# Kernel optimization log

Hardware: AMD Instinct MI355X
Metric: run time of the kernel (lower is better)

Reference implementation:

```python
import jax, jax.numpy as jnp
import numpy as np

B = 4096
D_IN = 1024
H1 = 2048
H2 = 1024
E = 7          # num_experts, forced by broadcasting in source
T = 2          # num_tasks
NS = 7         # scene dimension of S
EMB_ROWS = 10
EMB_DIM = 16


def setup_inputs() -> dict:
    key = jax.random.key(0)
    ks = jax.random.split(key, 8)
    x = jax.random.normal(ks[0], (B, D_IN), dtype=jnp.float32)
    scene = jax.random.randint(ks[1], (B,), 0, E)
    # Expert MLP params, stacked over experts: Linear(D_IN->H1)+ReLU, Linear(H1->H2)+ReLU
    W1 = jax.random.normal(ks[2], (E, D_IN, H1), dtype=jnp.float32) * (1.0 / np.sqrt(D_IN))
    b1 = jnp.zeros((E, H1), dtype=jnp.float32)
    W2 = jax.random.normal(ks[3], (E, H1, H2), dtype=jnp.float32) * (1.0 / np.sqrt(H1))
    b2 = jnp.zeros((E, H2), dtype=jnp.float32)
    # Routing tensor S: [7, input_dim+16, num_experts] (xavier-like init)
    S = jax.random.normal(ks[4], (NS, D_IN + EMB_DIM, E), dtype=jnp.float32) * 0.02
    scene_emb = jax.random.normal(ks[5], (EMB_ROWS, EMB_DIM), dtype=jnp.float32)
    return {"x": x, "scene": scene, "W1": W1, "b1": b1, "W2": W2, "b2": b2,
            "S": S, "scene_emb": scene_emb}


def _forward(x, scene, W1, b1, W2, b2, S, scene_emb):
    # Experts (vectorized over the E expert MLPs): [B,E,H2]
    h = jax.nn.relu(jnp.einsum('bd,edh->beh', x, W1) + b1)
    experts_out = jax.nn.relu(jnp.einsum('beh,eho->beo', h, W2) + b2)

    se = scene_emb[scene]                       # [B,16]
    xc = jnp.concatenate([x, se], axis=-1)      # [B, D_IN+16]
    G = jnp.einsum('bd,sde->bse', xc, S)        # [B, 7, E]
    G = jnp.transpose(G, (0, 2, 1))             # [B, E, 7]
    G = jax.nn.softmax(G, axis=-1)

    logG = jnp.log(G)                           # [B, E, 7]
    q = jnp.sum(jnp.log(G * 7.0) / 7.0, axis=-1)  # [B, E]

    KG = jnp.eye(E, dtype=x.dtype)
    ses = KG[scene][:, None, :]                 # [B, 1, E]

    _, pi = jax.lax.top_k(jnp.sum(ses * logG, axis=-1), 6)  # [B,6]
    _, qi = jax.lax.top_k(q, 6)                              # [B,6]
    select = ((KG[pi].sum(axis=1) + KG[qi].sum(axis=1)) > 0).astype(x.dtype)  # [B,E]

    gate = jax.nn.softmax(jnp.sum(G * ses, axis=-1), axis=-1) * select  # [B,E]
    out = jnp.einsum('be,bed->bd', gate, experts_out)                    # [B,H2]
    # self.gate ModuleList is unused in the source forward; each task output is identical
    return jnp.stack([out] * T, axis=0)         # [T, B, H2]


def reference(x, scene, W1, b1, W2, b2, S, scene_emb):
    return _forward(x, scene, W1, b1, W2, b2, S, scene_emb)
```

## Files before the change

### kernel.cpp

```cpp
#include <hip/hip_runtime.h>
#include <hip/hip_bf16.h>

typedef unsigned short u16;
typedef __bf16 bf8 __attribute__((ext_vector_type(8)));
typedef float f4 __attribute__((ext_vector_type(4)));

__device__ __forceinline__ u16 f2bf(float f) {
    unsigned int u = __float_as_uint(f);
    u = (u + 0x7fffu + ((u >> 16) & 1u)) >> 16;
    return (u16)u;
}

__device__ __forceinline__ void gload16(const u16* g, u16* l) {
    __builtin_amdgcn_global_load_lds((const __attribute__((address_space(1))) void*)g,
                                     (__attribute__((address_space(3))) void*)l, 16, 0, 0);
}

__global__ void transpose_cvt_kernel(const float* __restrict__ in, u16* __restrict__ out,
                                     int R, int C) {
    __shared__ u16 t[64][71];
    int e = blockIdx.z;
    int c0 = blockIdx.x * 64, r0 = blockIdx.y * 64;
    int tid = threadIdx.x;
    const float* ip = in + (size_t)e * R * C;
    u16* op = out + (size_t)e * R * C;
#pragma unroll
    for (int k = 0; k < 16; ++k) {
        int idx = k * 256 + tid;
        int r = idx >> 6, c = idx & 63;
        t[c][r] = f2bf(ip[(size_t)(r0 + r) * C + c0 + c]);
    }
    __syncthreads();
#pragma unroll
    for (int k = 0; k < 8; ++k) {
        int c = k * 8 + (tid >> 5);
        int rr = (tid & 31) * 2;
        ushort2 v = make_ushort2(t[c][rr], t[c][rr + 1]);
        *(ushort2*)(op + (size_t)(c0 + c) * R + r0 + rr) = v;
    }
}

__global__ void transpose_S_kernel(const float* __restrict__ S, float* __restrict__ ST) {
    int idx = blockIdx.x * 256 + threadIdx.x;
    if (idx >= 1040 * 52) return;
    int d = idx / 52, c = idx % 52;
    ST[idx] = (c < 49) ? S[(c / 7) * 7280 + d * 7 + (c % 7)] : 0.f;
}

__global__ void gating_kernel(const float* __restrict__ x, const int* __restrict__ scene,
                              const float* __restrict__ ST, const float* __restrict__ semb,
                              float* __restrict__ gate, u16* __restrict__ xb) {
    __shared__ float xc[4][1040];
    __shared__ float Lsh[4][49];
    int wv = threadIdx.x >> 6, lane = threadIdx.x & 63;
    int row = blockIdx.x * 4 + wv;
    float* xcw = xc[wv];
    const float* xr = x + (size_t)row * 1024;
    for (int d = lane; d < 1024; d += 64) xcw[d] = xr[d];
    int sc = scene[row];
    if (lane < 16) xcw[1024 + lane] = semb[sc * 16 + lane];
    __syncthreads();

    u16* xrow = xb + (size_t)row * 1024;
    for (int d = lane * 4; d < 1024; d += 256) {
        ushort4 o;
        o.x = f2bf(xcw[d]);     o.y = f2bf(xcw[d + 1]);
        o.z = f2bf(xcw[d + 2]); o.w = f2bf(xcw[d + 3]);
        *(ushort4*)(xrow + d) = o;
    }

    if (lane < 49) {
        const float* STp = ST + lane;
        float a0 = 0.f, a1 = 0.f, a2 = 0.f, a3 = 0.f;
        for (int d = 0; d < 1040; d += 4) {
            a0 += xcw[d]     * STp[d * 52];
            a1 += xcw[d + 1] * STp[d * 52 + 52];
            a2 += xcw[d + 2] * STp[d * 52 + 104];
            a3 += xcw[d + 3] * STp[d * 52 + 156];
        }
        Lsh[wv][lane] = (a0 + a1) + (a2 + a3);
    }
    __syncthreads();

    if (lane == 0) {
        float logG[7][7], Gsc[7], piS[7], qS[7];
        for (int e = 0; e < 7; e++) {
            float L[7];
            float m = -1e30f;
            for (int s = 0; s < 7; s++) { L[s] = Lsh[wv][s * 7 + e]; m = fmaxf(m, L[s]); }
            float sum = 0.f;
            for (int s = 0; s < 7; s++) sum += expf(L[s] - m);
            float lse = m + logf(sum);
            float qs = 0.f;
            for (int s = 0; s < 7; s++) { logG[e][s] = L[s] - lse; qs += logG[e][s]; }
            piS[e] = logG[e][sc];
            qS[e] = qs;
            Gsc[e] = expf(logG[e][sc]);
        }
        int epi = 0, eqi = 0; float bp = piS[0], bq = qS[0];
        for (int e = 1; e < 7; e++) {
            if (piS[e] <= bp) { bp = piS[e]; epi = e; }
            if (qS[e]  <= bq) { bq = qS[e];  eqi = e; }
        }
        float mg = -1e30f;
        for (int e = 0; e < 7; e++) mg = fmaxf(mg, Gsc[e]);
        float sum = 0.f;
        float ex[7];
        for (int e = 0; e < 7; e++) { ex[e] = expf(Gsc[e] - mg); sum += ex[e]; }
        float inv = 1.f / sum;
        for (int e = 0; e < 7; e++) {
            float g = ex[e] * inv;
            if (e == epi && e == eqi) g = 0.f;
            gate[row * 7 + e] = g;
        }
    }
}

template<bool G2>
__global__ __launch_bounds__(512, 2) void gemm8p_kernel(
    const u16* __restrict__ Abase, const u16* __restrict__ Bbase,
    const float* __restrict__ bias, const float* __restrict__ gate,
    void* __restrict__ outp)
{
    constexpr int M = 4096;
    constexpr int K = G2 ? 2048 : 1024;
    constexpr int N = G2 ? 1024 : 2048;
    constexpr int NT = K / 64;
    constexpr int LOG2NT = G2 ? 5 : 4;

    extern __shared__ u16 lds[];

    const int tid = threadIdx.x;
    const int lane = tid & 63;
    const int wid = tid >> 6;
    const int wr = wid >> 2, wc = wid & 3;
    const int ln15 = lane & 15, lnk = (lane >> 4) * 8;

    int bm, bn, e0, nE, grp;
    if constexpr (G2) {
        int id = blockIdx.x;
        int xcd = id & 7, slot = id >> 3;
        grp = xcd & 1;
        bn = slot & 3;
        bm = (slot >> 2) * 4 + (xcd >> 1);
        e0 = grp * 4; nE = grp ? 3 : 4;
    } else {
        int xcd = blockIdx.x & 7, slot = blockIdx.x >> 3;
        bn = slot >> 2;
        bm = (slot & 3) * 8 + xcd;
        e0 = 0; nE = 7; grp = 0;
    }
    const int NTtot = nE * NT;

    const int sr = tid >> 3;
    const int sc = (tid & 7) * 8;

    auto stageA = [&](int gt, int buf) {
#pragma unroll
        for (int l = 0; l < 2; ++l) {
            int r = l * 64 + sr;
            int cs = sc ^ ((r & 7) << 3);
            const u16* g = Abase + (G2 ? (size_t)(e0 + (gt >> LOG2NT)) * M * K : (size_t)0)
                         + (size_t)(bm * 128 + r) * K + (gt & (NT - 1)) * 64 + cs;
            gload16(g, lds + buf * 24576 + l * 4096 + tid * 8);
        }
    };
    auto stageB = [&](int gt, int buf, int h) {
#pragma unroll
        for (int l = 0; l < 2; ++l) {
            int rb = h * 128 + l * 64 + sr;
            int cs = sc ^ ((rb & 7) << 3);
            const u16* g = Bbase + (size_t)(e0 + (gt >> LOG2NT)) * N * K
                         + (size_t)(bn * 256 + rb) * K + (gt & (NT - 1)) * 64 + cs;
            gload16(g, lds + buf * 24576 + 8192 + h * 8192 + l * 4096 + tid * 8);
        }
    };
    auto aoff = [&](int mi, int ks) {
        int r = wr * 64 + mi * 16 + ln15;
        int c = ks * 32 + lnk;
        return r * 64 + (c ^ ((r & 7) << 3));
    };
    auto boff = [&](int ni, int ks) {
        int rb = wc * 64 + ni * 16 + ln15;
        int c = ks * 32 + lnk;
        return rb * 64 + (c ^ ((rb & 7) << 3));
    };

    f4 acc[4][4] = {};
    f4 fin[4][4] = {};
    bf8 aA[2][2], bL[2][2], bH[2][2];

    stageA(0, 0); stageB(0, 0, 0); stageB(0, 0, 1);

    for (int gt = 0; gt < NTtot; ++gt) {
        const int cur = gt & 1, nxt = cur ^ 1;
        const bool more = (gt + 1 < NTtot);
        const u16* Ac = lds + cur * 24576;
        const u16* Bc = lds + cur * 24576 + 8192;
        if (more) {
            stageA(gt + 1, nxt); stageB(gt + 1, nxt, 0);
            asm volatile("s_waitcnt vmcnt(4)" ::: "memory");
        } else {
            asm volatile("s_waitcnt vmcnt(0)" ::: "memory");
        }
        __builtin_amdgcn_sched_barrier(0);
        __builtin_amdgcn_s_barrier();
        __builtin_amdgcn_sched_barrier(0);
#pragma unroll
        for (int mi = 0; mi < 2; ++mi)
#pragma unroll
            for (int ks = 0; ks < 2; ++ks)
                aA[mi][ks] = *(const bf8*)(Ac + aoff(mi, ks));
#pragma unroll
        for (int ni = 0; ni < 2; ++ni)
#pragma unroll
            for (int ks = 0; ks < 2; ++ks)
                bL[ni][ks] = *(const bf8*)(Bc + boff(ni, ks));
        asm volatile("s_waitcnt lgkmcnt(0)" ::: "memory");
        __builtin_amdgcn_sched_barrier(0);
        __builtin_amdgcn_s_setprio(1);
#pragma unroll
        for (int mi = 0; mi < 2; ++mi)
#pragma unroll
            for (int ni = 0; ni < 2; ++ni)
#pragma unroll
                for (int ks = 0; ks < 2; ++ks)
                    acc[mi][ni] = __builtin_amdgcn_mfma_f32_16x16x32_bf16(aA[mi][ks], bL[ni][ks], acc[mi][ni], 0, 0, 0);
        __builtin_amdgcn_s_setprio(0);
        if (more) stageB(gt + 1, nxt, 1);
#pragma unroll
        for (int ni = 0; ni < 2; ++ni)
#pragma unroll
            for (int ks = 0; ks < 2; ++ks)
                bH[ni][ks] = *(const bf8*)(Bc + boff(2 + ni, ks));
        asm volatile("s_waitcnt lgkmcnt(0)" ::: "memory");
        __builtin_amdgcn_sched_barrier(0);
        __builtin_amdgcn_s_setprio(1);
#pragma unroll
        for (int mi = 0; mi < 2; ++mi)
#pragma unroll
            for (int ni = 0; ni < 2; ++ni)
#pragma unroll
                for (int ks = 0; ks < 2; ++ks)
                    acc[mi][2 + ni] = __builtin_amdgcn_mfma_f32_16x16x32_bf16(aA[mi][ks], bH[ni][ks], acc[mi][2 + ni], 0, 0, 0);
        __builtin_amdgcn_s_setprio(0);
#pragma unroll
        for (int mi = 0; mi < 2; ++mi)
#pragma unroll
            for (int ks = 0; ks < 2; ++ks)
                aA[mi][ks] = *(const bf8*)(Ac + aoff(2 + mi, ks));
        asm volatile("s_waitcnt lgkmcnt(0)" ::: "memory");
        __builtin_amdgcn_sched_barrier(0);
        __builtin_amdgcn_s_setprio(1);
#pragma unroll
        for (int mi = 0; mi < 2; ++mi)
#pragma unroll
            for (int ni = 0; ni < 2; ++ni)
#pragma unroll
                for (int ks = 0; ks < 2; ++ks)
                    acc[2 + mi][2 + ni] = __builtin_amdgcn_mfma_f32_16x16x32_bf16(aA[mi][ks], bH[ni][ks], acc[2 + mi][2 + ni], 0, 0, 0);
        __builtin_amdgcn_s_setprio(0);
        __builtin_amdgcn_sched_barrier(0);
        __builtin_amdgcn_s_barrier();
        __builtin_amdgcn_sched_barrier(0);
        __builtin_amdgcn_s_setprio(1);
#pragma unroll
        for (int mi = 0; mi < 2; ++mi)
#pragma unroll
            for (int ni = 0; ni < 2; ++ni)
#pragma unroll
                for (int ks = 0; ks < 2; ++ks)
                    acc[2 + mi][ni] = __builtin_amdgcn_mfma_f32_16x16x32_bf16(aA[mi][ks], bL[ni][ks], acc[2 + mi][ni], 0, 0, 0);
        __builtin_amdgcn_s_setprio(0);
        __builtin_amdgcn_sched_barrier(0);
        if ((gt & (NT - 1)) == NT - 1) {
            int e = e0 + (gt >> LOG2NT);
            float bloc[4];
#pragma unroll
            for (int ni = 0; ni < 4; ++ni)
                bloc[ni] = bias[e * N + bn * 256 + wc * 64 + ni * 16 + ln15];
            if constexpr (G2) {
#pragma unroll
                for (int mi = 0; mi < 4; ++mi)
#pragma unroll
                    for (int i = 0; i < 4; ++i) {
                        int row = bm * 128 + wr * 64 + mi * 16 + (lane >> 4) * 4 + i;
                        float g = gate[row * 7 + e];
#pragma unroll
                        for (int ni = 0; ni < 4; ++ni) {
                            fin[mi][ni][i] += g * fmaxf(acc[mi][ni][i] + bloc[ni], 0.f);
                            acc[mi][ni][i] = 0.f;
                        }
                    }
            } else {
                u16* Hp = (u16*)outp + (size_t)e * M * N;
#pragma unroll
                for (int mi = 0; mi < 4; ++mi)
#pragma unroll
                    for (int i = 0; i < 4; ++i) {
                        size_t row = (size_t)(bm * 128 + wr * 64 + mi * 16 + (lane >> 4) * 4 + i);
#pragma unroll
                        for (int ni = 0; ni < 4; ++ni) {
                            __builtin_nontemporal_store(
                                f2bf(fmaxf(acc[mi][ni][i] + bloc[ni], 0.f)),
                                &Hp[row * N + bn * 256 + wc * 64 + ni * 16 + ln15]);
                            acc[mi][ni][i] = 0.f;
                        }
                    }
            }
        }
    }

    if constexpr (G2) {
        float* po = (float*)outp + (size_t)grp * M * N;
#pragma unroll
        for (int mi = 0; mi < 4; ++mi)
#pragma unroll
            for (int i = 0; i < 4; ++i) {
                size_t row = (size_t)(bm * 128 + wr * 64 + mi * 16 + (lane >> 4) * 4 + i);
#pragma unroll
                for (int ni = 0; ni < 4; ++ni)
                    po[row * N + bn * 256 + wc * 64 + ni * 16 + ln15] = fin[mi][ni][i];
            }
    }
}

__global__ void combine_kernel(const float* __restrict__ p0, const float* __restrict__ p1,
                               float* __restrict__ out, int n4) {
    int i = blockIdx.x * blockDim.x + threadIdx.x;
    int stride = gridDim.x * blockDim.x;
    for (; i < n4; i += stride) {
        float4 a = ((const float4*)p0)[i];
        float4 b = ((const float4*)p1)[i];
        float4 v = make_float4(a.x + b.x, a.y + b.y, a.z + b.z, a.w + b.w);
        ((float4*)out)[i] = v;
        ((float4*)out)[i + n4] = v;
    }
}

extern "C" void kernel_launch(void* const* d_in, const int* in_sizes, int n_in,
                              void* d_out, int out_size, void* d_ws, size_t ws_size,
                              hipStream_t stream) {
    const float* x     = (const float*)d_in[0];
    const int*   scene = (const int*)d_in[1];
    const float* W1    = (const float*)d_in[2];
    const float* b1    = (const float*)d_in[3];
    const float* W2    = (const float*)d_in[4];
    const float* b2    = (const float*)d_in[5];
    const float* S     = (const float*)d_in[6];
    const float* semb  = (const float*)d_in[7];
    float* out = (float*)d_out;

    char* ws = (char*)d_ws;
    float* part = (float*)(ws);
    u16*   xb   = (u16*)(ws);
    u16*   W1T  = (u16*)(ws + 8388608);
    u16*   W2T  = (u16*)(ws + 37748736);
    u16*   Hb   = (u16*)(ws + 67108864);
    float* gate = (float*)(ws + 184549376);
    float* ST   = (float*)(ws + 184664064);

    (void)hipFuncSetAttribute(reinterpret_cast<const void*>(gemm8p_kernel<false>),
                              hipFuncAttributeMaxDynamicSharedMemorySize, 98304);
    (void)hipFuncSetAttribute(reinterpret_cast<const void*>(gemm8p_kernel<true>),
                              hipFuncAttributeMaxDynamicSharedMemorySize, 98304);

    transpose_cvt_kernel<<<dim3(32, 16, 7), 256, 0, stream>>>(W1, W1T, 1024, 2048);
    transpose_cvt_kernel<<<dim3(16, 32, 7), 256, 0, stream>>>(W2, W2T, 2048, 1024);
    transpose_S_kernel<<<(1040 * 52 + 255) / 256, 256, 0, stream>>>(S, ST);
    gating_kernel<<<1024, 256, 0, stream>>>(x, scene, ST, semb, gate, xb);
    gemm8p_kernel<false><<<256, 512, 98304, stream>>>(xb, W1T, b1, nullptr, Hb);
    gemm8p_kernel<true><<<256, 512, 98304, stream>>>(Hb, W2T, b2, gate, part);
    combine_kernel<<<2048, 256, 0, stream>>>(part, part + 4096 * 1024, out, 4096 * 1024 / 4);
}
```

Measured before the change: 360.2 us.

## Fuse split-K combine into second GEMM via flag-synchronized partial sums

Removes the separate combine kernel. The group-0 blocks of the second GEMM write their partial results and then set a per-tile flag. The group-1 blocks spin on that flag, add the partial in registers, and write both task copies directly to the output. The expert split is rebalanced to 3/4 so the waiting group carries more work, and the flags are cleared by a memset before launch. This saves one launch and a full read/write pass over the partials, at the cost of inter-block spin-waits that depend on co-residency of the producer blocks.

After: 358.4 us. No clear change (-0.5%).

```diff
diff --git a/kernel.cpp b/kernel.cpp
--- a/kernel.cpp
+++ b/kernel.cpp
@@ -120,7 +120,7 @@
 __global__ __launch_bounds__(512, 2) void gemm8p_kernel(
     const u16* __restrict__ Abase, const u16* __restrict__ Bbase,
     const float* __restrict__ bias, const float* __restrict__ gate,
-    void* __restrict__ outp)
+    void* __restrict__ outp, float* __restrict__ part, int* __restrict__ flags)
 {
     constexpr int M = 4096;
     constexpr int K = G2 ? 2048 : 1024;
@@ -143,7 +143,7 @@
         grp = xcd & 1;
         bn = slot & 3;
         bm = (slot >> 2) * 4 + (xcd >> 1);
-        e0 = grp * 4; nE = grp ? 3 : 4;
+        e0 = grp ? 3 : 0; nE = grp ? 4 : 3;
     } else {
         int xcd = blockIdx.x & 7, slot = blockIdx.x >> 3;
         bn = slot >> 2;
@@ -312,29 +312,45 @@
     }
 
     if constexpr (G2) {
-        float* po = (float*)outp + (size_t)grp * M * N;
-#pragma unroll
-        for (int mi = 0; mi < 4; ++mi)
-#pragma unroll
-            for (int i = 0; i < 4; ++i) {
-                size_t row = (size_t)(bm * 128 + wr * 64 + mi * 16 + (lane >> 4) * 4 + i);
-#pragma unroll
-                for (int ni = 0; ni < 4; ++ni)
-                    po[row * N + bn * 256 + wc * 64 + ni * 16 + ln15] = fin[mi][ni][i];
+        const int fi = bm * 4 + bn;
+        if (grp == 0) {
+#pragma unroll
+            for (int mi = 0; mi < 4; ++mi)
+#pragma unroll
+                for (int i = 0; i < 4; ++i) {
+                    size_t row = (size_t)(bm * 128 + wr * 64 + mi * 16 + (lane >> 4) * 4 + i);
+#pragma unroll
+                    for (int ni = 0; ni < 4; ++ni)
+                        __hip_atomic_store(&part[row * N + bn * 256 + wc * 64 + ni * 16 + ln15],
+                                           fin[mi][ni][i],
+                                           __ATOMIC_RELAXED, __HIP_MEMORY_SCOPE_AGENT);
+                }
+            __syncthreads();
+            if (tid == 0)
+                __hip_atomic_store(&flags[fi], 1, __ATOMIC_RELEASE, __HIP_MEMORY_SCOPE_AGENT);
+        } else {
+            if (tid == 0) {
+                while (__hip_atomic_load(&flags[fi], __ATOMIC_ACQUIRE, __HIP_MEMORY_SCOPE_AGENT) == 0)
+                    __builtin_amdgcn_s_sleep(8);
             }
-    }
-}
-
-__global__ void combine_kernel(const float* __restrict__ p0, const float* __restrict__ p1,
-                               float* __restrict__ out, int n4) {
-    int i = blockIdx.x * blockDim.x + threadIdx.x;
-    int stride = gridDim.x * blockDim.x;
-    for (; i < n4; i += stride) {
-        float4 a = ((const float4*)p0)[i];
-        float4 b = ((const float4*)p1)[i];
-        float4 v = make_float4(a.x + b.x, a.y + b.y, a.z + b.z, a.w + b.w);
-        ((float4*)out)[i] = v;
-        ((float4*)out)[i + n4] = v;
+            __syncthreads();
+            float* out0 = (float*)outp;
+#pragma unroll
+            for (int mi = 0; mi < 4; ++mi)
+#pragma unroll
+                for (int i = 0; i < 4; ++i) {
+                    size_t row = (size_t)(bm * 128 + wr * 64 + mi * 16 + (lane >> 4) * 4 + i);
+#pragma unroll
+                    for (int ni = 0; ni < 4; ++ni) {
+                        size_t idx = row * N + bn * 256 + wc * 64 + ni * 16 + ln15;
+                        float v = fin[mi][ni][i] +
+                                  __hip_atomic_load(&part[idx], __ATOMIC_RELAXED,
+                                                    __HIP_MEMORY_SCOPE_AGENT);
+                        out0[idx] = v;
+                        out0[(size_t)M * N + idx] = v;
+                    }
+                }
+        }
     }
 }
 
@@ -352,13 +368,15 @@
     float* out = (float*)d_out;
 
     char* ws = (char*)d_ws;
-    float* part = (float*)(ws);
-    u16*   xb   = (u16*)(ws);
-    u16*   W1T  = (u16*)(ws + 8388608);
-    u16*   W2T  = (u16*)(ws + 37748736);
-    u16*   Hb   = (u16*)(ws + 67108864);
-    float* gate = (float*)(ws + 184549376);
-    float* ST   = (float*)(ws + 184664064);
+    float* part  = (float*)(ws);
+    u16*   xb    = (u16*)(ws);
+    u16*   W1T   = (u16*)(ws + 8388608);
+    int*   flags = (int*)(ws + 16777216 + 20971520);
+    u16*   W2T   = (u16*)(ws + 37748736);
+    u16*   Hb    = (u16*)(ws + 67108864);
+    float* gate  = (float*)(ws + 184549376);
+    float* ST    = (float*)(ws + 184664064);
+    flags        = (int*)(ws + 16777216);
 
     (void)hipFuncSetAttribute(reinterpret_cast<const void*>(gemm8p_kernel<false>),
                               hipFuncAttributeMaxDynamicSharedMemorySize, 98304);
@@ -369,7 +387,7 @@
     transpose_cvt_kernel<<<dim3(16, 32, 7), 256, 0, stream>>>(W2, W2T, 2048, 1024);
     transpose_S_kernel<<<(1040 * 52 + 255) / 256, 256, 0, stream>>>(S, ST);
     gating_kernel<<<1024, 256, 0, stream>>>(x, scene, ST, semb, gate, xb);
-    gemm8p_kernel<false><<<256, 512, 98304, stream>>>(xb, W1T, b1, nullptr, Hb);
-    gemm8p_kernel<true><<<256, 512, 98304, stream>>>(Hb, W2T, b2, gate, part);
-    combine_kernel<<<2048, 256, 0, stream>>>(part, part + 4096 * 1024, out, 4096 * 1024 / 4);
-}
+    gemm8p_kernel<false><<<256, 512, 98304, stream>>>(xb, W1T, b1, nullptr, Hb, nullptr, nullptr);
+    (void)hipMemsetAsync(flags, 0, 512, stream);
+    gemm8p_kernel<true><<<256, 512, 98304, stream>>>(Hb, W2T, b2, gate, out, part, flags);
+}
```
